# Kernel tuning notes

Measured on AMD Instinct MI355X. Metric: run time of the kernel, lower is better.

Reference implementation:

```python
import jax, jax.numpy as jnp
import numpy as np

B, S, D, H = 4, 2048, 1024, 16
DK = D // H


def setup_inputs() -> dict:
    key = jax.random.key(0)
    ks = jax.random.split(key, 11)
    std = 1.0 / np.sqrt(D)
    mk = lambda k: jax.random.uniform(k, (D, D), jnp.float32, -std, std)
    mb = lambda k: jax.random.uniform(k, (D,), jnp.float32, -std, std)
    return {
        "query": jax.random.normal(ks[0], (B, S, D), jnp.float32),
        "key": jax.random.normal(ks[1], (B, S, D), jnp.float32),
        "value": jax.random.normal(ks[2], (B, S, D), jnp.float32),
        "Wq": mk(ks[3]), "bq": mb(ks[4]),
        "Wk": mk(ks[5]), "bk": mb(ks[6]),
        "Wv": mk(ks[7]), "bv": mb(ks[8]),
        "Wo": mk(ks[9]), "bo": mb(ks[10]),
    }


def reference(query, key, value, Wq, bq, Wk, bk, Wv, bv, Wo, bo):
    # Linear projections (torch Linear: x @ W.T + b)
    Q = query @ Wq.T + bq   # [B,S,D]
    K = key @ Wk.T + bk
    V = value @ Wv.T + bv
    # split heads -> [B,H,S,DK]
    Q = Q.reshape(B, S, H, DK).transpose(0, 2, 1, 3)
    K = K.reshape(B, S, H, DK).transpose(0, 2, 1, 3)
    V = V.reshape(B, S, H, DK).transpose(0, 2, 1, 3)
    scale = 1.0 / jnp.sqrt(jnp.asarray(DK, Q.dtype))
    scores = jnp.einsum("bhqd,bhkd->bhqk", Q, K) * scale  # [B,H,S,S]
    attn = jax.nn.softmax(scores, axis=-1)
    out = jnp.einsum("bhqk,bhkd->bhqd", attn, V)          # [B,H,S,DK]
    out = out.transpose(0, 2, 1, 3).reshape(B, S, D)       # [B,S,D]
    return out @ Wo.T + bo
```

## Files before the change

### kernel.cpp

```cpp
#include <hip/hip_runtime.h>
#include <hip/hip_bf16.h>
#include <stdint.h>


using f32x4  = __attribute__((ext_vector_type(4))) float;
using f32x16 = __attribute__((ext_vector_type(16))) float;
using s16x8  = __attribute__((ext_vector_type(8))) short;
using u16x8  = __attribute__((ext_vector_type(8))) unsigned short;
using u16x4  = __attribute__((ext_vector_type(4))) unsigned short;

#define MFMA16(a, b, c) __builtin_amdgcn_mfma_f32_16x16x32_bf16((a), (b), (c), 0, 0, 0)
#define MFMA32(a, b, c) __builtin_amdgcn_mfma_f32_32x32x16_bf16((a), (b), (c), 0, 0, 0)

#define GLL16(gptr, lptr)                                                      \
  __builtin_amdgcn_global_load_lds(                                            \
      (const __attribute__((address_space(1))) void*)(gptr),                   \
      (__attribute__((address_space(3))) void*)(lptr), 16, 0, 0)

__device__ __forceinline__ unsigned short f2bf(float f) {
  union { __hip_bfloat16 h; unsigned short u; } cv;
  cv.h = __float2bfloat16(f);
  return cv.u;
}

__device__ __forceinline__ unsigned int pkrne(float a, float b) {
  unsigned int ua = __builtin_bit_cast(unsigned int, a);
  unsigned int ub = __builtin_bit_cast(unsigned int, b);
  ua = ua + 0x7FFFu + ((ua >> 16) & 1u);
  ub = ub + 0x7FFFu + ((ub >> 16) & 1u);
  return (ua >> 16) | (ub & 0xFFFF0000u);
}

__device__ __forceinline__ float exp2a(float x) {
  return __builtin_amdgcn_exp2f(x);
}

__global__ __launch_bounds__(256) void cast_w_kernel(
    const float* __restrict__ wq, const float* __restrict__ wk,
    const float* __restrict__ wv, const float* __restrict__ wo,
    unsigned short* __restrict__ dst) {
  int i = blockIdx.x * 256 + threadIdx.x;
  int m = i >> 18;
  int off = i & 0x3FFFF;
  const float* src = (m == 0) ? wq : (m == 1) ? wk : (m == 2) ? wv : wo;
  float4 v = reinterpret_cast<const float4*>(src)[off];
  u16x4 o;
  o[0] = f2bf(v.x); o[1] = f2bf(v.y); o[2] = f2bf(v.z); o[3] = f2bf(v.w);
  *reinterpret_cast<u16x4*>(dst + (size_t)i * 4) = o;
}

__global__ __launch_bounds__(256) void gemm_qkv_kernel(
    const float* __restrict__ xq, const float* __restrict__ xk, const float* __restrict__ xv,
    const unsigned short* __restrict__ wbf,
    const float* __restrict__ bq, const float* __restrict__ bk, const float* __restrict__ bv,
    unsigned short* __restrict__ Qh, unsigned short* __restrict__ Kh,
    unsigned short* __restrict__ Vh) {
  const int z = blockIdx.z;
  const float* X = (z == 0) ? xq : (z == 1) ? xk : xv;
  const float* bias = (z == 0) ? bq : (z == 1) ? bk : bv;
  const unsigned short* W = wbf + (size_t)z * 1048576;
  unsigned short* dst = (z == 0) ? Qh : (z == 1) ? Kh : Vh;
  const float qscale = (z == 0) ? 0.18033688011112042f : 1.0f;

  __shared__ __align__(16) unsigned short Ab[128 * 64];
  __shared__ __align__(16) unsigned short Bs[128 * 64];

  const int t = threadIdx.x;
  const int lane = t & 63, w = t >> 6;
  const int g = lane >> 4, c = lane & 15;
  const int wm = (w >> 1) * 64, wn = (w & 1) * 64;
  const int n0 = (blockIdx.y & 7) * 128;
  const int m0 = (blockIdx.x * 8 + (blockIdx.y >> 3)) * 128;

  f32x4 acc[4][4];
#pragma unroll
  for (int i = 0; i < 4; i++)
#pragma unroll
    for (int j = 0; j < 4; j++) acc[i][j] = (f32x4)0.0f;

  const int arow_lo = t >> 4;
  const int af0 = (t & 15) * 4;
  const int alc = (t & 15) >> 1;
  const int ah = (t & 15) & 1;
  const int blr = lane >> 3;
  const int bgc = (lane & 7) ^ blr;

  for (int kt = 0; kt < 16; ++kt) {
    const int k0 = kt * 64;
    __syncthreads();
#pragma unroll
    for (int i = 0; i < 4; i++) {
      int ii = w * 4 + i;
      const unsigned short* gsrc = W + (size_t)(n0 + ii * 8 + blr) * 1024 + k0 + bgc * 8;
      GLL16(gsrc, &Bs[ii * 512]);
    }
#pragma unroll
    for (int j = 0; j < 8; j++) {
      int r = j * 16 + arow_lo;
      float4 v = *reinterpret_cast<const float4*>(X + (size_t)(m0 + r) * 1024 + k0 + af0);
      uint2 p;
      p.x = pkrne(v.x, v.y);
      p.y = pkrne(v.z, v.w);
      int pc = alc ^ (r & 7);
      *reinterpret_cast<uint2*>(&Ab[r * 64 + pc * 8 + ah * 4]) = p;
    }
    __syncthreads();

#pragma unroll
    for (int ks = 0; ks < 2; ks++) {
      s16x8 af[4], bfr[4];
#pragma unroll
      for (int mt = 0; mt < 4; mt++) {
        int r = wm + mt * 16 + c;
        af[mt] = *reinterpret_cast<const s16x8*>(&Ab[r * 64 + (((ks * 4 + g) ^ (c & 7)) << 3)]);
      }
#pragma unroll
      for (int nt = 0; nt < 4; nt++) {
        int r = wn + nt * 16 + c;
        bfr[nt] = *reinterpret_cast<const s16x8*>(&Bs[r * 64 + (((ks * 4 + g) ^ (c & 7)) << 3)]);
      }
#pragma unroll
      for (int mt = 0; mt < 4; mt++)
#pragma unroll
        for (int nt = 0; nt < 4; nt++)
          acc[mt][nt] = MFMA16(af[mt], bfr[nt], acc[mt][nt]);
    }
  }

#pragma unroll
  for (int mt = 0; mt < 4; mt++)
#pragma unroll
    for (int nt = 0; nt < 4; nt++) {
      int n = n0 + wn + nt * 16 + c;
      float bb = bias[n];
      int h = n >> 6, dk = n & 63;
#pragma unroll
      for (int r = 0; r < 4; r++) {
        int m = m0 + wm + mt * 16 + g * 4 + r;
        int b = m >> 11, s = m & 2047;
        dst[(((size_t)b * 16 + h) * 2048 + s) * 64 + dk] =
            f2bf((acc[mt][nt][r] + bb) * qscale);
      }
    }
}

__global__ __launch_bounds__(256) void gemm_out_kernel(
    const unsigned short* __restrict__ AO, const unsigned short* __restrict__ Wo,
    const float* __restrict__ bo, float* __restrict__ out) {
  __shared__ __align__(16) unsigned short Asm_[128 * 64];
  __shared__ __align__(16) unsigned short Bsm_[128 * 64];

  const int t = threadIdx.x;
  const int lane = t & 63, w = t >> 6;
  const int g = lane >> 4, c = lane & 15;
  const int wm = (w >> 1) * 64, wn = (w & 1) * 64;
  const int n0 = (blockIdx.y & 7) * 128;
  const int m0 = (blockIdx.x * 8 + (blockIdx.y >> 3)) * 128;

  f32x4 acc[4][4];
#pragma unroll
  for (int i = 0; i < 4; i++)
#pragma unroll
    for (int j = 0; j < 4; j++) acc[i][j] = (f32x4)0.0f;

  const int blr = lane >> 3;
  const int bgc = (lane & 7) ^ blr;

  for (int kt = 0; kt < 16; ++kt) {
    const int k0 = kt * 64;
    __syncthreads();
#pragma unroll
    for (int i = 0; i < 4; i++) {
      int ii = w * 4 + i;
      const unsigned short* ga = AO + (size_t)(m0 + ii * 8 + blr) * 1024 + k0 + bgc * 8;
      GLL16(ga, &Asm_[ii * 512]);
      const unsigned short* gb = Wo + (size_t)(n0 + ii * 8 + blr) * 1024 + k0 + bgc * 8;
      GLL16(gb, &Bsm_[ii * 512]);
    }
    __syncthreads();

#pragma unroll
    for (int ks = 0; ks < 2; ks++) {
      s16x8 af[4], bfr[4];
#pragma unroll
      for (int mt = 0; mt < 4; mt++) {
        int r = wm + mt * 16 + c;
        af[mt] = *reinterpret_cast<const s16x8*>(&Asm_[r * 64 + (((ks * 4 + g) ^ (c & 7)) << 3)]);
      }
#pragma unroll
      for (int nt = 0; nt < 4; nt++) {
        int r = wn + nt * 16 + c;
        bfr[nt] = *reinterpret_cast<const s16x8*>(&Bsm_[r * 64 + (((ks * 4 + g) ^ (c & 7)) << 3)]);
      }
#pragma unroll
      for (int mt = 0; mt < 4; mt++)
#pragma unroll
        for (int nt = 0; nt < 4; nt++)
          acc[mt][nt] = MFMA16(af[mt], bfr[nt], acc[mt][nt]);
    }
  }

#pragma unroll
  for (int mt = 0; mt < 4; mt++)
#pragma unroll
    for (int nt = 0; nt < 4; nt++) {
      int n = n0 + wn + nt * 16 + c;
      float bb = bo[n];
#pragma unroll
      for (int r = 0; r < 4; r++) {
        int m = m0 + wm + mt * 16 + g * 4 + r;
        out[(size_t)m * 1024 + n] = acc[mt][nt][r] + bb;
      }
    }
}

__global__ __launch_bounds__(512) void attn_kernel(
    const unsigned short* __restrict__ Qh, const unsigned short* __restrict__ Kh,
    const unsigned short* __restrict__ Vh, unsigned short* __restrict__ AO) {
  const int bh = blockIdx.x * 8 + (blockIdx.y >> 3);
  const int b = bh >> 4, h = bh & 15;
  const int q0 = (blockIdx.y & 7) * 256;
  const int t = threadIdx.x, lane = t & 63, w = t >> 6;
  const int lo = lane & 31, hi = lane >> 5;

  __shared__ __align__(16) unsigned short Ks[2][64 * 64];
  __shared__ __align__(16) unsigned short Vt[2][64 * 64];

  const size_t kvbase = (size_t)bh * 2048 * 64;

  s16x8 qb[4];
  {
    const unsigned short* qp = Qh + kvbase + (size_t)(q0 + w * 32 + lo) * 64;
#pragma unroll
    for (int ks = 0; ks < 4; ks++)
      qb[ks] = *reinterpret_cast<const s16x8*>(qp + ks * 16 + hi * 8);
  }

  f32x16 oacc[2];
  oacc[0] = (f32x16)0.0f; oacc[1] = (f32x16)0.0f;
  float lsum = 0.0f;

  const int skrow = t >> 3, sks = t & 7;
  const int kgc = sks ^ (skrow & 7) ^ w;
  const int vkrow = t >> 3, vd0 = (t & 7) * 8;
  const int vwc = w ^ (t & 7);
  const int vcl = vkrow & 7;

  const int rx0 = (lo & 7) ^ (lo >> 3);
  const int rx1 = (lo & 7) ^ (4 | (lo >> 3));

  uint4 kk, vv;
  kk = *reinterpret_cast<const uint4*>(Kh + kvbase + (size_t)skrow * 64 + kgc * 8);
  vv = *reinterpret_cast<const uint4*>(Vh + kvbase + (size_t)vkrow * 64 + vd0);
  *reinterpret_cast<uint4*>(&Ks[0][(size_t)t * 8]) = kk;
  {
    const unsigned short* vs = reinterpret_cast<const unsigned short*>(&vv);
#pragma unroll
    for (int j = 0; j < 8; j++)
      Vt[0][(vd0 + j) * 64 + ((vwc ^ j) << 3) + vcl] = vs[j];
  }

  for (int it = 0; it < 32; ++it) {
    const int cur = it & 1, nxt = cur ^ 1;
    const bool more = (it < 31);
    if (more) {
      const int kv = (it + 1) * 64;
      kk = *reinterpret_cast<const uint4*>(Kh + kvbase + (size_t)(kv + skrow) * 64 + kgc * 8);
      vv = *reinterpret_cast<const uint4*>(Vh + kvbase + (size_t)(kv + vkrow) * 64 + vd0);
    }
    __syncthreads();

    f32x16 st[2];
    st[0] = (f32x16)0.0f; st[1] = (f32x16)0.0f;
#pragma unroll
    for (int kb = 0; kb < 2; kb++) {
      const int rx = kb ? rx1 : rx0;
#pragma unroll
      for (int ks = 0; ks < 4; ks++) {
        s16x8 ka = *reinterpret_cast<const s16x8*>(
            &Ks[cur][(kb * 32 + lo) * 64 + (((ks * 2 + hi) ^ rx) << 3)]);
        st[kb] = MFMA32(ka, qb[ks], st[kb]);
      }
    }

    s16x8 pa[4];
    float s0 = 0.0f, s1 = 0.0f, s2 = 0.0f, s3 = 0.0f;
#pragma unroll
    for (int kb = 0; kb < 2; kb++) {
      float e[16];
#pragma unroll
      for (int r = 0; r < 16; r += 4) {
        e[r]     = exp2a(st[kb][r]);
        e[r + 1] = exp2a(st[kb][r + 1]);
        e[r + 2] = exp2a(st[kb][r + 2]);
        e[r + 3] = exp2a(st[kb][r + 3]);
        s0 += e[r]; s1 += e[r + 1]; s2 += e[r + 2]; s3 += e[r + 3];
      }
#pragma unroll
      for (int half = 0; half < 2; half++) {
        const float* eb = e + half * 8;
        unsigned int x1 = pkrne(eb[0], eb[1]);
        unsigned int x2 = pkrne(eb[2], eb[3]);
        unsigned int y1 = pkrne(eb[4], eb[5]);
        unsigned int y2 = pkrne(eb[6], eb[7]);
        asm volatile("v_permlane32_swap_b32 %0, %1" : "+v"(x1), "+v"(y1));
        asm volatile("v_permlane32_swap_b32 %0, %1" : "+v"(x2), "+v"(y2));
        uint4 u;
        u.x = x1; u.y = x2; u.z = y1; u.w = y2;
        pa[kb * 2 + half] = *reinterpret_cast<const s16x8*>(&u);
      }
    }
    lsum += (s0 + s1) + (s2 + s3);

    if (more) {
      *reinterpret_cast<uint4*>(&Ks[nxt][(size_t)t * 8]) = kk;
      const unsigned short* vs = reinterpret_cast<const unsigned short*>(&vv);
#pragma unroll
      for (int j = 0; j < 8; j++)
        Vt[nxt][(vd0 + j) * 64 + ((vwc ^ j) << 3) + vcl] = vs[j];
    }

#pragma unroll
    for (int ks = 0; ks < 4; ks++)
#pragma unroll
      for (int db = 0; db < 2; db++) {
        const int rx = db ? rx1 : rx0;
        s16x8 vb = *reinterpret_cast<const s16x8*>(
            &Vt[cur][(db * 32 + lo) * 64 + (((ks * 2 + hi) ^ rx) << 3)]);
        oacc[db] = MFMA32(pa[ks], vb, oacc[db]);
      }
  }

  float ltot = lsum + __shfl_xor(lsum, 32);
  float linv = 1.0f / ltot;
#pragma unroll
  for (int r = 0; r < 16; r++) {
    int qr = (r & 3) + ((r >> 2) << 3) + (hi << 2);
    float inv_r = __shfl(linv, qr);
    int srow = q0 + w * 32 + qr;
    size_t obase = ((size_t)b * 2048 + srow) * 1024 + (size_t)h * 64;
    AO[obase + lo]      = f2bf(oacc[0][r] * inv_r);
    AO[obase + 32 + lo] = f2bf(oacc[1][r] * inv_r);
  }
}

extern "C" void kernel_launch(void* const* d_in, const int* in_sizes, int n_in,
                              void* d_out, int out_size, void* d_ws, size_t ws_size,
                              hipStream_t stream) {
  const float* query = (const float*)d_in[0];
  const float* key   = (const float*)d_in[1];
  const float* value = (const float*)d_in[2];
  const float* Wq = (const float*)d_in[3];
  const float* bq = (const float*)d_in[4];
  const float* Wk = (const float*)d_in[5];
  const float* bk = (const float*)d_in[6];
  const float* Wv = (const float*)d_in[7];
  const float* bv = (const float*)d_in[8];
  const float* Wo = (const float*)d_in[9];
  const float* bo = (const float*)d_in[10];

  uint8_t* wsb = (uint8_t*)d_ws;
  unsigned short* wbf = (unsigned short*)wsb;
  unsigned short* Qh  = (unsigned short*)(wsb + 8388608);
  unsigned short* Kh  = (unsigned short*)(wsb + 8388608 + 16777216);
  unsigned short* Vh  = (unsigned short*)(wsb + 8388608 + 2 * 16777216);
  unsigned short* AO  = (unsigned short*)(wsb + 8388608 + 3 * 16777216);

  cast_w_kernel<<<dim3(4096), dim3(256), 0, stream>>>(Wq, Wk, Wv, Wo, wbf);
  gemm_qkv_kernel<<<dim3(8, 64, 3), dim3(256), 0, stream>>>(
      query, key, value, wbf, bq, bk, bv, Qh, Kh, Vh);
  attn_kernel<<<dim3(8, 64), dim3(512), 0, stream>>>(Qh, Kh, Vh, AO);
  gemm_out_kernel<<<dim3(8, 64), dim3(256), 0, stream>>>(
      AO, wbf + (size_t)3 * 1048576, bo, (float*)d_out);
}
```

Measured before the change: 218.9 us.

## Pre-cast activations to bf16 and split QKV GEMM into per-projection launches

Adds a separate kernel that casts each fp32 input activation to bf16 into a reused workspace buffer. The QKV GEMM then loads the A tile with direct global-to-LDS loads, the same path already used for the weights, instead of loading fp32 into registers, converting and writing to LDS. Because the bf16 buffer is shared, the single batched launch becomes three cast+GEMM pairs run in sequence. This simplifies the GEMM's load path but adds an extra round trip of the activations through memory, four more launches, and a smaller grid per GEMM launch.

```diff
diff --git a/kernel.cpp b/kernel.cpp
--- a/kernel.cpp
+++ b/kernel.cpp
@@ -49,21 +49,22 @@
   *reinterpret_cast<u16x4*>(dst + (size_t)i * 4) = o;
 }
 
-__global__ __launch_bounds__(256) void gemm_qkv_kernel(
-    const float* __restrict__ xq, const float* __restrict__ xk, const float* __restrict__ xv,
-    const unsigned short* __restrict__ wbf,
-    const float* __restrict__ bq, const float* __restrict__ bk, const float* __restrict__ bv,
-    unsigned short* __restrict__ Qh, unsigned short* __restrict__ Kh,
-    unsigned short* __restrict__ Vh) {
-  const int z = blockIdx.z;
-  const float* X = (z == 0) ? xq : (z == 1) ? xk : xv;
-  const float* bias = (z == 0) ? bq : (z == 1) ? bk : bv;
-  const unsigned short* W = wbf + (size_t)z * 1048576;
-  unsigned short* dst = (z == 0) ? Qh : (z == 1) ? Kh : Vh;
-  const float qscale = (z == 0) ? 0.18033688011112042f : 1.0f;
-
-  __shared__ __align__(16) unsigned short Ab[128 * 64];
-  __shared__ __align__(16) unsigned short Bs[128 * 64];
+__global__ __launch_bounds__(256) void cast_x_kernel(
+    const float* __restrict__ src, unsigned short* __restrict__ dst) {
+  int i = blockIdx.x * 256 + threadIdx.x;
+  float4 v = reinterpret_cast<const float4*>(src)[i];
+  uint2 p;
+  p.x = pkrne(v.x, v.y);
+  p.y = pkrne(v.z, v.w);
+  *reinterpret_cast<uint2*>(dst + (size_t)i * 4) = p;
+}
+
+__global__ __launch_bounds__(256) void gemm_qkvz_kernel(
+    const unsigned short* __restrict__ Xbf, const unsigned short* __restrict__ W,
+    const float* __restrict__ bias, unsigned short* __restrict__ dst,
+    float qscale) {
+  __shared__ __align__(16) unsigned short Asm_[128 * 64];
+  __shared__ __align__(16) unsigned short Bsm_[128 * 64];
 
   const int t = threadIdx.x;
   const int lane = t & 63, w = t >> 6;
@@ -78,10 +79,6 @@
 #pragma unroll
     for (int j = 0; j < 4; j++) acc[i][j] = (f32x4)0.0f;
 
-  const int arow_lo = t >> 4;
-  const int af0 = (t & 15) * 4;
-  const int alc = (t & 15) >> 1;
-  const int ah = (t & 15) & 1;
   const int blr = lane >> 3;
   const int bgc = (lane & 7) ^ blr;
 
@@ -91,18 +88,10 @@
 #pragma unroll
     for (int i = 0; i < 4; i++) {
       int ii = w * 4 + i;
-      const unsigned short* gsrc = W + (size_t)(n0 + ii * 8 + blr) * 1024 + k0 + bgc * 8;
-      GLL16(gsrc, &Bs[ii * 512]);
-    }
-#pragma unroll
-    for (int j = 0; j < 8; j++) {
-      int r = j * 16 + arow_lo;
-      float4 v = *reinterpret_cast<const float4*>(X + (size_t)(m0 + r) * 1024 + k0 + af0);
-      uint2 p;
-      p.x = pkrne(v.x, v.y);
-      p.y = pkrne(v.z, v.w);
-      int pc = alc ^ (r & 7);
-      *reinterpret_cast<uint2*>(&Ab[r * 64 + pc * 8 + ah * 4]) = p;
+      const unsigned short* ga = Xbf + (size_t)(m0 + ii * 8 + blr) * 1024 + k0 + bgc * 8;
+      GLL16(ga, &Asm_[ii * 512]);
+      const unsigned short* gb = W + (size_t)(n0 + ii * 8 + blr) * 1024 + k0 + bgc * 8;
+      GLL16(gb, &Bsm_[ii * 512]);
     }
     __syncthreads();
 
@@ -112,12 +101,12 @@
 #pragma unroll
       for (int mt = 0; mt < 4; mt++) {
         int r = wm + mt * 16 + c;
-        af[mt] = *reinterpret_cast<const s16x8*>(&Ab[r * 64 + (((ks * 4 + g) ^ (c & 7)) << 3)]);
+        af[mt] = *reinterpret_cast<const s16x8*>(&Asm_[r * 64 + (((ks * 4 + g) ^ (c & 7)) << 3)]);
       }
 #pragma unroll
       for (int nt = 0; nt < 4; nt++) {
         int r = wn + nt * 16 + c;
-        bfr[nt] = *reinterpret_cast<const s16x8*>(&Bs[r * 64 + (((ks * 4 + g) ^ (c & 7)) << 3)]);
+        bfr[nt] = *reinterpret_cast<const s16x8*>(&Bsm_[r * 64 + (((ks * 4 + g) ^ (c & 7)) << 3)]);
       }
 #pragma unroll
       for (int mt = 0; mt < 4; mt++)
@@ -365,10 +354,22 @@
   unsigned short* Kh  = (unsigned short*)(wsb + 8388608 + 16777216);
   unsigned short* Vh  = (unsigned short*)(wsb + 8388608 + 2 * 16777216);
   unsigned short* AO  = (unsigned short*)(wsb + 8388608 + 3 * 16777216);
+  unsigned short* Xbf = AO;
+
+  const float QSCALE = 0.18033688011112042f;
 
   cast_w_kernel<<<dim3(4096), dim3(256), 0, stream>>>(Wq, Wk, Wv, Wo, wbf);
-  gemm_qkv_kernel<<<dim3(8, 64, 3), dim3(256), 0, stream>>>(
-      query, key, value, wbf, bq, bk, bv, Qh, Kh, Vh);
+
+  cast_x_kernel<<<dim3(8192), dim3(256), 0, stream>>>(query, Xbf);
+  gemm_qkvz_kernel<<<dim3(8, 64), dim3(256), 0, stream>>>(
+      Xbf, wbf + (size_t)0 * 1048576, bq, Qh, QSCALE);
+  cast_x_kernel<<<dim3(8192), dim3(256), 0, stream>>>(key, Xbf);
+  gemm_qkvz_kernel<<<dim3(8, 64), dim3(256), 0, stream>>>(
+      Xbf, wbf + (size_t)1 * 1048576, bk, Kh, 1.0f);
+  cast_x_kernel<<<dim3(8192), dim3(256), 0, stream>>>(value, Xbf);
+  gemm_qkvz_kernel<<<dim3(8, 64), dim3(256), 0, stream>>>(
+      Xbf, wbf + (size_t)2 * 1048576, bv, Vh, 1.0f);
+
   attn_kernel<<<dim3(8, 64), dim3(512), 0, stream>>>(Qh, Kh, Vh, AO);
   gemm_out_kernel<<<dim3(8, 64), dim3(256), 0, stream>>>(
       AO, wbf + (size_t)3 * 1048576, bo, (float*)d_out);
```

Measured after the change: 229.5 us. +4.9%, slower.
